# Performance work log

Measured on AMD Instinct MI355X. Metric: run time of the kernel, lower is better.

## Reference

```python
import jax, jax.numpy as jnp
import numpy as np


def setup_inputs() -> dict:
    key = jax.random.key(0)
    ks = jax.random.split(key, 8)
    B, C, W, H = 4, 256, 64, 64
    dqk = C // 8
    s_in = 1.0 / np.sqrt(C)
    return {
        "x": jax.random.normal(ks[0], (B, C, W, H), dtype=jnp.float32),
        "Wq": jax.random.normal(ks[1], (dqk, C), dtype=jnp.float32) * s_in,
        "bq": jnp.zeros((dqk,), dtype=jnp.float32),
        "Wk": jax.random.normal(ks[2], (dqk, C), dtype=jnp.float32) * s_in,
        "bk": jnp.zeros((dqk,), dtype=jnp.float32),
        "Wv": jax.random.normal(ks[3], (C, C), dtype=jnp.float32) * s_in,
        "bv": jnp.zeros((C,), dtype=jnp.float32),
        "gamma": jnp.zeros((1,), dtype=jnp.float32),
    }


def reference(x, Wq, bq, Wk, bk, Wv, bv, gamma):
    B, C, W, H = x.shape
    N = W * H
    xf = x.reshape(B, C, N)  # flatten spatial: B x C x N
    # 1x1 convs == per-pixel linear projections over channels
    q = jnp.einsum("bcn,dc->bnd", xf, Wq) + bq            # B x N x dqk
    k = jnp.einsum("bcn,dc->bdn", xf, Wk) + bk[None, :, None]  # B x dqk x N
    v = jnp.einsum("bcn,dc->bdn", xf, Wv) + bv[None, :, None]  # B x C x N
    # unscaled attention, softmax over keys (last dim)
    attn = jax.nn.softmax(jnp.einsum("bnd,bdm->bnm", q, k), axis=-1)  # B x N x N
    # out[b,c,i] = sum_j v[b,c,j] * attn[b,i,j]  (bmm with attn^T)
    out = jnp.einsum("bcj,bij->bci", v, attn).reshape(B, C, W, H)
    return gamma[0] * out + x
```

## Files before the change

### kernel.cpp

```cpp
#include <hip/hip_runtime.h>

#define BB 4
#define CC 256
#define NN 4096

typedef __attribute__((ext_vector_type(8))) short bh8;
typedef __attribute__((ext_vector_type(4))) float f32x4;

#define WPK_OFF  0
#define BALL_OFF 163840
#define QBF_OFF  165888
#define KBF_OFF  (165888 + 1048576)
#define VBF_OFF  (165888 + 2097152)

typedef const __attribute__((address_space(1))) void* gas_t;
typedef __attribute__((address_space(3))) void* las_t;
__device__ inline void gld16(const void* g, void* l) {
    __builtin_amdgcn_global_load_lds((gas_t)g, (las_t)l, 16, 0, 0);
}

__device__ inline int pack2bf(float a, float b) {
    unsigned ua = __builtin_bit_cast(unsigned, a) + 0x8000u;
    unsigned ub = __builtin_bit_cast(unsigned, b) + 0x8000u;
    return (int)__builtin_amdgcn_perm(ub, ua, 0x07060302u);
}
__device__ inline short f2bf1(float a) {
    return (short)((__builtin_bit_cast(unsigned, a) + 0x8000u) >> 16);
}

__global__ __launch_bounds__(256) void prep_w(const float* __restrict__ Wq,
        const float* __restrict__ bq, const float* __restrict__ Wk,
        const float* __restrict__ bk, const float* __restrict__ Wv,
        const float* __restrict__ bv, short* __restrict__ Wpk,
        float* __restrict__ ball) {
    int tid = blockIdx.x * 256 + threadIdx.x;
    if (tid < 10240) {
        int lane = tid & 63;
        int fc = tid >> 6;
        int mt = fc >> 3, ck = fc & 7;
        int m = mt * 16 + (lane & 15);
        int c0 = ck * 32 + (lane >> 4) * 8;
        const float* wrow;
        if (m < 32)      wrow = Wq + m * 256;
        else if (m < 64) wrow = Wk + (m - 32) * 256;
        else             wrow = Wv + (m - 64) * 256;
        int d[4];
        #pragma unroll
        for (int p = 0; p < 4; ++p)
            d[p] = pack2bf(wrow[c0 + 2 * p], wrow[c0 + 2 * p + 1]);
        *(int4*)(Wpk + tid * 8) = make_int4(d[0], d[1], d[2], d[3]);
    }
    if (tid < 320) {
        float b2 = tid < 32 ? bq[tid] : (tid < 64 ? bk[tid - 32] : bv[tid - 64]);
        ball[tid] = b2;
    }
}

__global__ __launch_bounds__(256) void proj(const float* __restrict__ x,
        const short* __restrict__ Wpk, const float* __restrict__ ball,
        short* __restrict__ qbf, short* __restrict__ kbf,
        short* __restrict__ vbf) {
    int t = threadIdx.x;
    int w = t >> 6, lane = t & 63, quad = lane >> 4, c15 = lane & 15;
    int gw = blockIdx.x * 4 + w;
    int tile = gw >> 1, mh = gw & 1;
    int b = tile >> 8, n0 = (tile & 255) * 16;
    const float* xb = x + (size_t)b * CC * NN;

    bh8 af[8];
    #pragma unroll
    for (int ck = 0; ck < 8; ++ck) {
        float v[8];
        #pragma unroll
        for (int e = 0; e < 8; ++e)
            v[e] = xb[(size_t)(ck * 32 + quad * 8 + e) * NN + n0 + c15];
        int d[4];
        #pragma unroll
        for (int p = 0; p < 4; ++p) d[p] = pack2bf(v[2 * p], v[2 * p + 1]);
        af[ck] = __builtin_bit_cast(bh8, make_int4(d[0], d[1], d[2], d[3]));
    }

    #pragma unroll
    for (int mpi = 0; mpi < 5; ++mpi) {
        int mp = mh * 5 + mpi;
        int mtA = mp * 2, mtB = mp * 2 + 1;
        float blA = ball[mtA * 16 + c15], blB = ball[mtB * 16 + c15];
        f32x4 accA = {blA, blA, blA, blA}, accB = {blB, blB, blB, blB};
        #pragma unroll
        for (int ck = 0; ck < 8; ++ck) {
            bh8 wfA = *(const bh8*)(Wpk + ((mtA * 8 + ck) * 64 + lane) * 8);
            bh8 wfB = *(const bh8*)(Wpk + ((mtB * 8 + ck) * 64 + lane) * 8);
            accA = __builtin_amdgcn_mfma_f32_16x16x32_bf16(af[ck], wfA, accA, 0, 0, 0);
            accB = __builtin_amdgcn_mfma_f32_16x16x32_bf16(af[ck], wfB, accB, 0, 0, 0);
        }
        #pragma unroll
        for (int half = 0; half < 2; ++half) {
            int mt = mp * 2 + half;
            f32x4 acc = half ? accB : accA;
            if (mt < 4) {
                short* dst = (mt < 2) ? qbf : kbf;
                int m = (mt & 1) * 16 + c15;
                #pragma unroll
                for (int r = 0; r < 4; ++r)
                    dst[(size_t)(b * NN + n0 + quad * 4 + r) * 32 + m] = f2bf1(acc[r]);
            } else {
                int c = mt * 16 + c15 - 64;
                int2 pk;
                pk.x = pack2bf(acc[0], acc[1]);
                pk.y = pack2bf(acc[2], acc[3]);
                *(int2*)(vbf + (size_t)b * CC * NN + (size_t)c * NN + n0 + quad * 4) = pk;
            }
        }
    }
}

__global__ __launch_bounds__(512, 2) void flash_attn(
        const short* __restrict__ qbf, const short* __restrict__ kbf,
        const short* __restrict__ vbf, const float* __restrict__ x,
        const float* __restrict__ gamma, float* __restrict__ out) {
    __shared__ char lds[82944];

    int bid = blockIdx.x;
    int b = bid & 3, i0 = (bid >> 2) * 64;
    int t = threadIdx.x;
    int w = t >> 6, lane = t & 63, quad = lane >> 4, c15 = lane & 15;
    int mg = w & 3, nh = w >> 2, jsub = w & 3;

    const short* qb = qbf + (size_t)b * NN * 32;
    const short* kb = kbf + (size_t)b * NN * 32;
    const short* vb = vbf + (size_t)b * CC * NN;

    bh8 qf0 = *(const bh8*)(qb + (size_t)(i0 + nh * 32 + c15) * 32 + quad * 8);
    bh8 qf1 = *(const bh8*)(qb + (size_t)(i0 + nh * 32 + 16 + c15) * 32 + quad * 8);

    int vrow = w * 32 + (lane >> 3);
    int glog = (lane & 7) ^ ((lane >> 3) & 7);
    const short* vsg = vb + (size_t)vrow * NN + glog * 8;
    char* vdst = lds + w * 4096;

    const short* kptr = kb + (size_t)(jsub * 16 + c15) * 32 + quad * 8;

    char* Pt = lds + 65536;
    float* lred = (float*)(lds + 81920);

    f32x4 acc[4][2];
    #pragma unroll
    for (int ms = 0; ms < 4; ++ms) {
        acc[ms][0] = (f32x4){0.f, 0.f, 0.f, 0.f};
        acc[ms][1] = (f32x4){0.f, 0.f, 0.f, 0.f};
    }
    float lsum0 = 0.f, lsum1 = 0.f;
    const f32x4 initc = {-12.f, -12.f, -12.f, -12.f};

    #pragma unroll
    for (int r = 0; r < 4; ++r) gld16(vsg + r * 8 * NN, vdst + r * 1024);
    bh8 kf = *(const bh8*)kptr;
    __syncthreads();

    for (int jt = 0; jt < 64; ++jt) {
        int cur = jt & 1;
        f32x4 sa0 = __builtin_amdgcn_mfma_f32_16x16x32_bf16(kf, qf0, initc, 0, 0, 0);
        f32x4 sa1 = __builtin_amdgcn_mfma_f32_16x16x32_bf16(kf, qf1, initc, 0, 0, 0);
        bh8 kfn = *(const bh8*)(kptr + (size_t)((jt + 1) & 63) * 2048);
        float p0[4], p1[4];
        #pragma unroll
        for (int r = 0; r < 4; ++r) {
            p0[r] = __expf(sa0[r]); lsum0 += p0[r];
            p1[r] = __expf(sa1[r]); lsum1 += p1[r];
        }
        char* Ptc = Pt + cur * 8192;
        int g = jsub * 2 + (quad >> 1);
        int pb0 = (nh * 32 + c15) * 128 + ((g ^ (c15 & 7)) * 16) + (quad & 1) * 8;
        *(int2*)(Ptc + pb0) = make_int2(pack2bf(p0[0], p0[1]), pack2bf(p0[2], p0[3]));
        *(int2*)(Ptc + pb0 + 2048) = make_int2(pack2bf(p1[0], p1[1]), pack2bf(p1[2], p1[3]));

        __syncthreads();

        if (jt < 63) {
            const short* vs = vsg + (jt + 1) * 64;
            char* vd = vdst + ((cur ^ 1) << 15);
            #pragma unroll
            for (int r = 0; r < 4; ++r) gld16(vs + r * 8 * NN, vd + r * 1024);
        }

        const char* Vb = lds + cur * 32768;
        #pragma unroll
        for (int kk = 0; kk < 2; ++kk) {
            int gs = ((kk * 4 + quad) ^ (c15 & 7)) * 16;
            bh8 pfa = *(const bh8*)(Ptc + (nh * 32 + c15) * 128 + gs);
            bh8 pfb = *(const bh8*)(Ptc + (nh * 32 + 16 + c15) * 128 + gs);
            #pragma unroll
            for (int ms = 0; ms < 4; ++ms) {
                int c = mg * 64 + ms * 16 + c15;
                bh8 vf = *(const bh8*)(Vb + c * 128 + gs);
                acc[ms][0] = __builtin_amdgcn_mfma_f32_16x16x32_bf16(vf, pfa, acc[ms][0], 0, 0, 0);
                acc[ms][1] = __builtin_amdgcn_mfma_f32_16x16x32_bf16(vf, pfb, acc[ms][1], 0, 0, 0);
            }
        }
        kf = kfn;
    }

    lsum0 += __shfl_xor(lsum0, 16); lsum0 += __shfl_xor(lsum0, 32);
    lsum1 += __shfl_xor(lsum1, 16); lsum1 += __shfl_xor(lsum1, 32);
    __syncthreads();
    if (lane < 16) {
        lred[w * 32 + lane] = lsum0;
        lred[w * 32 + 16 + lane] = lsum1;
    }
    __syncthreads();
    float l0 = lred[(nh * 4 + 0) * 32 + c15] + lred[(nh * 4 + 1) * 32 + c15]
             + lred[(nh * 4 + 2) * 32 + c15] + lred[(nh * 4 + 3) * 32 + c15];
    float l1 = lred[(nh * 4 + 0) * 32 + 16 + c15] + lred[(nh * 4 + 1) * 32 + 16 + c15]
             + lred[(nh * 4 + 2) * 32 + 16 + c15] + lred[(nh * 4 + 3) * 32 + 16 + c15];
    float linv0 = 1.0f / l0, linv1 = 1.0f / l1;

    float gm = gamma[0];
    const float* xb2 = x + (size_t)b * CC * NN;
    float* ob = out + (size_t)b * CC * NN;
    int ia = i0 + nh * 32 + c15, ib2 = ia + 16;
    #pragma unroll
    for (int ms = 0; ms < 4; ++ms) {
        #pragma unroll
        for (int r = 0; r < 4; ++r) {
            int c = mg * 64 + ms * 16 + quad * 4 + r;
            ob[(size_t)c * NN + ia]  = gm * acc[ms][0][r] * linv0 + xb2[(size_t)c * NN + ia];
            ob[(size_t)c * NN + ib2] = gm * acc[ms][1][r] * linv1 + xb2[(size_t)c * NN + ib2];
        }
    }
}

extern "C" void kernel_launch(void* const* d_in, const int* in_sizes, int n_in,
                              void* d_out, int out_size, void* d_ws, size_t ws_size,
                              hipStream_t stream) {
    const float* x     = (const float*)d_in[0];
    const float* Wq    = (const float*)d_in[1];
    const float* bq    = (const float*)d_in[2];
    const float* Wk    = (const float*)d_in[3];
    const float* bk    = (const float*)d_in[4];
    const float* Wv    = (const float*)d_in[5];
    const float* bv    = (const float*)d_in[6];
    const float* gamma = (const float*)d_in[7];
    float* out = (float*)d_out;
    char*  ws  = (char*)d_ws;
    short* Wpk  = (short*)(ws + WPK_OFF);
    float* ball = (float*)(ws + BALL_OFF);
    short* qbf  = (short*)(ws + QBF_OFF);
    short* kbf  = (short*)(ws + KBF_OFF);
    short* vbf  = (short*)(ws + VBF_OFF);

    prep_w<<<40, 256, 0, stream>>>(Wq, bq, Wk, bk, Wv, bv, Wpk, ball);
    proj<<<512, 256, 0, stream>>>(x, Wpk, ball, qbf, kbf, vbf);
    flash_attn<<<256, 512, 0, stream>>>(qbf, kbf, vbf, x, gamma, out);
}
```

Measured before the change: 142.4 us.

## Halve attention query tile and split projection output work across more waves

The attention kernel now handles 32 queries per 256-thread block instead of 64 per 512-thread block. Each wave computes all 32 query rows for its own 64 output channels and loads twice as many V rows per step. The launch doubles to 512 blocks, the P tile shrinks, and the row-sum reduction buffer now reuses the P area so one barrier can be dropped. The projection kernel now spreads each 16-pixel tile across 5 waves instead of 2, giving more waves in flight. The cost is that the attention kernel reads V twice as often in total, and each x tile is loaded and converted 5 times instead of 2.

```diff
diff --git a/kernel.cpp b/kernel.cpp
--- a/kernel.cpp
+++ b/kernel.cpp
@@ -63,7 +63,7 @@
     int t = threadIdx.x;
     int w = t >> 6, lane = t & 63, quad = lane >> 4, c15 = lane & 15;
     int gw = blockIdx.x * 4 + w;
-    int tile = gw >> 1, mh = gw & 1;
+    int tile = gw / 5, mh = gw % 5;
     int b = tile >> 8, n0 = (tile & 255) * 16;
     const float* xb = x + (size_t)b * CC * NN;
 
@@ -81,8 +81,8 @@
     }
 
     #pragma unroll
-    for (int mpi = 0; mpi < 5; ++mpi) {
-        int mp = mh * 5 + mpi;
+    for (int mpi = 0; mpi < 2; ++mpi) {
+        int mp = mh * 2 + mpi;
         int mtA = mp * 2, mtB = mp * 2 + 1;
         float blA = ball[mtA * 16 + c15], blB = ball[mtB * 16 + c15];
         f32x4 accA = {blA, blA, blA, blA}, accB = {blB, blB, blB, blB};
@@ -114,34 +114,33 @@
     }
 }
 
-__global__ __launch_bounds__(512, 2) void flash_attn(
+__global__ __launch_bounds__(256, 2) void flash_attn(
         const short* __restrict__ qbf, const short* __restrict__ kbf,
         const short* __restrict__ vbf, const float* __restrict__ x,
         const float* __restrict__ gamma, float* __restrict__ out) {
-    __shared__ char lds[82944];
+    __shared__ char lds[73728];
 
     int bid = blockIdx.x;
-    int b = bid & 3, i0 = (bid >> 2) * 64;
+    int b = bid & 3, i0 = (bid >> 2) * 32;
     int t = threadIdx.x;
     int w = t >> 6, lane = t & 63, quad = lane >> 4, c15 = lane & 15;
-    int mg = w & 3, nh = w >> 2, jsub = w & 3;
+    int jsub = w;
 
     const short* qb = qbf + (size_t)b * NN * 32;
     const short* kb = kbf + (size_t)b * NN * 32;
     const short* vb = vbf + (size_t)b * CC * NN;
 
-    bh8 qf0 = *(const bh8*)(qb + (size_t)(i0 + nh * 32 + c15) * 32 + quad * 8);
-    bh8 qf1 = *(const bh8*)(qb + (size_t)(i0 + nh * 32 + 16 + c15) * 32 + quad * 8);
-
-    int vrow = w * 32 + (lane >> 3);
+    bh8 qf0 = *(const bh8*)(qb + (size_t)(i0 + c15) * 32 + quad * 8);
+    bh8 qf1 = *(const bh8*)(qb + (size_t)(i0 + 16 + c15) * 32 + quad * 8);
+
+    int vrow = w * 64 + (lane >> 3);
     int glog = (lane & 7) ^ ((lane >> 3) & 7);
     const short* vsg = vb + (size_t)vrow * NN + glog * 8;
-    char* vdst = lds + w * 4096;
+    char* vdst = lds + w * 8192;
 
     const short* kptr = kb + (size_t)(jsub * 16 + c15) * 32 + quad * 8;
 
     char* Pt = lds + 65536;
-    float* lred = (float*)(lds + 81920);
 
     f32x4 acc[4][2];
     #pragma unroll
@@ -153,7 +152,7 @@
     const f32x4 initc = {-12.f, -12.f, -12.f, -12.f};
 
     #pragma unroll
-    for (int r = 0; r < 4; ++r) gld16(vsg + r * 8 * NN, vdst + r * 1024);
+    for (int r = 0; r < 8; ++r) gld16(vsg + r * 8 * NN, vdst + r * 1024);
     bh8 kf = *(const bh8*)kptr;
     __syncthreads();
 
@@ -168,9 +167,9 @@
             p0[r] = __expf(sa0[r]); lsum0 += p0[r];
             p1[r] = __expf(sa1[r]); lsum1 += p1[r];
         }
-        char* Ptc = Pt + cur * 8192;
+        char* Ptc = Pt + cur * 4096;
         int g = jsub * 2 + (quad >> 1);
-        int pb0 = (nh * 32 + c15) * 128 + ((g ^ (c15 & 7)) * 16) + (quad & 1) * 8;
+        int pb0 = c15 * 128 + ((g ^ (c15 & 7)) * 16) + (quad & 1) * 8;
         *(int2*)(Ptc + pb0) = make_int2(pack2bf(p0[0], p0[1]), pack2bf(p0[2], p0[3]));
         *(int2*)(Ptc + pb0 + 2048) = make_int2(pack2bf(p1[0], p1[1]), pack2bf(p1[2], p1[3]));
 
@@ -180,18 +179,18 @@
             const short* vs = vsg + (jt + 1) * 64;
             char* vd = vdst + ((cur ^ 1) << 15);
             #pragma unroll
-            for (int r = 0; r < 4; ++r) gld16(vs + r * 8 * NN, vd + r * 1024);
+            for (int r = 0; r < 8; ++r) gld16(vs + r * 8 * NN, vd + r * 1024);
         }
 
         const char* Vb = lds + cur * 32768;
         #pragma unroll
         for (int kk = 0; kk < 2; ++kk) {
             int gs = ((kk * 4 + quad) ^ (c15 & 7)) * 16;
-            bh8 pfa = *(const bh8*)(Ptc + (nh * 32 + c15) * 128 + gs);
-            bh8 pfb = *(const bh8*)(Ptc + (nh * 32 + 16 + c15) * 128 + gs);
+            bh8 pfa = *(const bh8*)(Ptc + c15 * 128 + gs);
+            bh8 pfb = *(const bh8*)(Ptc + (16 + c15) * 128 + gs);
             #pragma unroll
             for (int ms = 0; ms < 4; ++ms) {
-                int c = mg * 64 + ms * 16 + c15;
+                int c = w * 64 + ms * 16 + c15;
                 bh8 vf = *(const bh8*)(Vb + c * 128 + gs);
                 acc[ms][0] = __builtin_amdgcn_mfma_f32_16x16x32_bf16(vf, pfa, acc[ms][0], 0, 0, 0);
                 acc[ms][1] = __builtin_amdgcn_mfma_f32_16x16x32_bf16(vf, pfb, acc[ms][1], 0, 0, 0);
@@ -202,27 +201,27 @@
 
     lsum0 += __shfl_xor(lsum0, 16); lsum0 += __shfl_xor(lsum0, 32);
     lsum1 += __shfl_xor(lsum1, 16); lsum1 += __shfl_xor(lsum1, 32);
-    __syncthreads();
+    float* lred = (float*)Pt;
     if (lane < 16) {
         lred[w * 32 + lane] = lsum0;
         lred[w * 32 + 16 + lane] = lsum1;
     }
     __syncthreads();
-    float l0 = lred[(nh * 4 + 0) * 32 + c15] + lred[(nh * 4 + 1) * 32 + c15]
-             + lred[(nh * 4 + 2) * 32 + c15] + lred[(nh * 4 + 3) * 32 + c15];
-    float l1 = lred[(nh * 4 + 0) * 32 + 16 + c15] + lred[(nh * 4 + 1) * 32 + 16 + c15]
-             + lred[(nh * 4 + 2) * 32 + 16 + c15] + lred[(nh * 4 + 3) * 32 + 16 + c15];
+    float l0 = lred[0 * 32 + c15] + lred[1 * 32 + c15]
+             + lred[2 * 32 + c15] + lred[3 * 32 + c15];
+    float l1 = lred[0 * 32 + 16 + c15] + lred[1 * 32 + 16 + c15]
+             + lred[2 * 32 + 16 + c15] + lred[3 * 32 + 16 + c15];
     float linv0 = 1.0f / l0, linv1 = 1.0f / l1;
 
     float gm = gamma[0];
     const float* xb2 = x + (size_t)b * CC * NN;
     float* ob = out + (size_t)b * CC * NN;
-    int ia = i0 + nh * 32 + c15, ib2 = ia + 16;
+    int ia = i0 + c15, ib2 = i0 + 16 + c15;
     #pragma unroll
     for (int ms = 0; ms < 4; ++ms) {
         #pragma unroll
         for (int r = 0; r < 4; ++r) {
-            int c = mg * 64 + ms * 16 + quad * 4 + r;
+            int c = w * 64 + ms * 16 + quad * 4 + r;
             ob[(size_t)c * NN + ia]  = gm * acc[ms][0][r] * linv0 + xb2[(size_t)c * NN + ia];
             ob[(size_t)c * NN + ib2] = gm * acc[ms][1][r] * linv1 + xb2[(size_t)c * NN + ib2];
         }
@@ -249,6 +248,6 @@
     short* vbf  = (short*)(ws + VBF_OFF);
 
     prep_w<<<40, 256, 0, stream>>>(Wq, bq, Wk, bk, Wv, bv, Wpk, ball);
-    proj<<<512, 256, 0, stream>>>(x, Wpk, ball, qbf, kbf, vbf);
-    flash_attn<<<256, 512, 0, stream>>>(qbf, kbf, vbf, x, gamma, out);
-}
+    proj<<<1280, 256, 0, stream>>>(x, Wpk, ball, qbf, kbf, vbf);
+    flash_attn<<<512, 256, 0, stream>>>(qbf, kbf, vbf, x, gamma, out);
+}
```

Measured after the change: 160.8 us. 1.13x slower.
